# Kernel tuning notes

Measured on AMD Instinct MI355X. Metric: run time of the kernel, lower is better.

## Reference

```python
import jax, jax.numpy as jnp
import numpy as np

EPS = 1e-6
K = 20
NEG_SLOPE = 0.2

def knn_idx(x, k):
    # x: (B, D, N) flattened vector features; returns (B, N, k) neighbor indices
    inner = -2.0 * jnp.einsum('bdn,bdm->bnm', x, x)
    xx = jnp.sum(x * x, axis=1)  # (B, N)
    pd = -xx[:, :, None] - inner - xx[:, None, :]  # negative squared distance
    _, idx = jax.lax.top_k(pd, k)
    return idx

def get_graph_feature(x, k):
    # x: (B, C, 3, N) -> (B, 2C, 3, N, k) edge features (nbr - ctr, ctr)
    B, C, _, N = x.shape
    idx = knn_idx(x.reshape(B, C * 3, N), k)           # (B, N, k)
    feat = jnp.transpose(x, (0, 3, 1, 2))              # (B, N, C, 3)
    nb = jax.vmap(lambda f, i: f[i])(feat, idx)        # (B, N, k, C, 3)
    ctr = jnp.broadcast_to(feat[:, :, None], nb.shape)
    out = jnp.concatenate([nb - ctr, ctr], axis=3)     # (B, N, k, 2C, 3)
    return jnp.transpose(out, (0, 3, 4, 1, 2))

def vn_batchnorm(x, gamma, beta):
    # x: (B, C, 3, ...); BatchNorm (training stats) applied to vector norms
    norm = jnp.linalg.norm(x, axis=2) + EPS            # (B, C, ...)
    axes = (0,) + tuple(range(2, norm.ndim))
    mu = jnp.mean(norm, axis=axes, keepdims=True)
    var = jnp.var(norm, axis=axes, keepdims=True)
    shape = (1, -1) + (1,) * (norm.ndim - 2)
    nbn = (norm - mu) / jnp.sqrt(var + 1e-5) * gamma.reshape(shape) + beta.reshape(shape)
    return x / norm[:, :, None] * nbn[:, :, None]

def vn_linear_leakyrelu(x, w_feat, w_dir, gamma, beta):
    # x: (B, Cin, 3, ...) -> (B, Cout, 3, ...)
    p = jnp.einsum('oc,bc...->bo...', w_feat, x)
    p = vn_batchnorm(p, gamma, beta)
    d = jnp.einsum('oc,bc...->bo...', w_dir, x)
    dot = jnp.sum(p * d, axis=2, keepdims=True)
    dsq = jnp.sum(d * d, axis=2, keepdims=True)
    proj = p - (dot / (dsq + EPS)) * d
    return NEG_SLOPE * p + (1.0 - NEG_SLOPE) * jnp.where(dot >= 0, p, proj)

def _forward(x, w1, d1, g1, b1, w2, d2, g2, b2, w3, d3, g3, b3, w4, d4, g4, b4, w5, d5, g5, b5):
    h = jnp.transpose(x, (0, 2, 1))[:, None]           # (B, 1, 3, N)
    h = vn_linear_leakyrelu(get_graph_feature(h, K), w1, d1, g1, b1)
    x1 = jnp.mean(h, axis=-1)                          # mean_pool over k: (B, 21, 3, N)
    h = vn_linear_leakyrelu(get_graph_feature(x1, K), w2, d2, g2, b2)
    x2 = jnp.mean(h, axis=-1)                          # (B, 21, 3, N)
    h = vn_linear_leakyrelu(get_graph_feature(x2, K), w3, d3, g3, b3)
    x3 = jnp.mean(h, axis=-1)                          # (B, 42, 3, N)
    h = vn_linear_leakyrelu(get_graph_feature(x3, K), w4, d4, g4, b4)
    x4 = jnp.mean(h, axis=-1)                          # (B, 85, 3, N)
    cat = jnp.concatenate([x1, x2, x3, x4], axis=1)    # (B, 169, 3, N)
    return vn_linear_leakyrelu(cat, w5, d5, g5, b5)    # (B, 341, 3, N)

def setup_inputs():
    key = jax.random.key(0)
    B, N = 8, 1024
    d = {"x": jax.random.normal(key, (B, N, 3), dtype=jnp.float32)}
    feat_shapes = {"1": (21, 2), "2": (21, 42), "3": (42, 42), "4": (85, 84), "5": (341, 169)}
    dir_out = {"1": 21, "2": 21, "3": 42, "4": 85, "5": 1}  # conv5 shares nonlinearity -> 1 dir channel
    for i, (name, (co, ci)) in enumerate(feat_shapes.items()):
        k1, k2 = jax.random.split(jax.random.fold_in(key, i + 1))
        s = 1.0 / np.sqrt(ci)
        d["w" + name] = jax.random.uniform(k1, (co, ci), minval=-s, maxval=s, dtype=jnp.float32)
        d["d" + name] = jax.random.uniform(k2, (dir_out[name], ci), minval=-s, maxval=s, dtype=jnp.float32)
        d["g" + name] = jnp.ones((co,), dtype=jnp.float32)
        d["b" + name] = jnp.zeros((co,), dtype=jnp.float32)
    return d

def reference(x, w1, d1, g1, b1, w2, d2, g2, b2, w3, d3, g3, b3, w4, d4, g4, b4, w5, d5, g5, b5):
    return _forward(x, w1, d1, g1, b1, w2, d2, g2, b2, w3, d3, g3, b3, w4, d4, g4, b4, w5, d5, g5, b5)
```

## Files before the change

kernel.cpp:

```cpp
#include <hip/hip_runtime.h>
#include <math.h>

#define KNN 20
#define NS 0.2f
#define EPSV 1e-6f
#define QT 4
#define OT 8
#define CROW 507
#define SSPLIT 8

struct F3 { float x, y, z; };

extern __shared__ __align__(16) float smem[];

__global__ void k_transpose(const float* __restrict__ x, float* __restrict__ xt,
                            float* __restrict__ xx, int B, int N) {
    int i = blockIdx.x * blockDim.x + threadIdx.x;
    if (i >= B * N) return;
    int b = i / N, n = i % N;
    const float* src = x + (size_t)(b * N + n) * 3;
    float* dst = xt + (size_t)b * 3 * N + n;
    float s0 = src[0], s1 = src[1], s2 = src[2];
    dst[0] = s0;
    dst[(size_t)N] = s1;
    dst[(size_t)2 * N] = s2;
    float s = 0.f;
    s += s0 * s0;
    s += s1 * s1;
    s += s2 * s2;
    xx[i] = s;
}

__global__ void k_sqnorm(const float* __restrict__ X, float* __restrict__ xx,
                         int N, int D, long batchStride, long sliceOff) {
    int i = blockIdx.x * 256 + threadIdx.x;
    int b = i / N, n = i % N;
    const float* Xb = X + (size_t)b * batchStride + sliceOff + n;
    float s = 0.f;
    for (int d = 0; d < D; ++d) {
        float v = Xb[(size_t)d * N];
        s += v * v;
    }
    xx[i] = s;
}

__global__ void k_knn(const float* __restrict__ X, const float* __restrict__ xx,
                      int* __restrict__ idx,
                      int N, int D, long batchStride, long sliceOff) {
    int b = blockIdx.y;
    int q0 = blockIdx.x * QT;
    int tid = threadIdx.x;
    int lane = tid & 63;
    int wave = tid >> 6;

    __shared__ __align__(16) float qf[128 * QT];
    __shared__ __align__(16) float pd[QT][1024];

    const float* Xb = X + (size_t)b * batchStride + sliceOff;
    const float* xxb = xx + (size_t)b * N;

    for (int t = tid; t < QT * D; t += 256) {
        int d = t >> 2, q = t & 3;
        qf[d * QT + q] = Xb[(size_t)d * N + (q0 + q)];
    }
    __syncthreads();

    float a0x = 0.f, a0y = 0.f, a0z = 0.f, a0w = 0.f;
    float a1x = 0.f, a1y = 0.f, a1z = 0.f, a1w = 0.f;
    float a2x = 0.f, a2y = 0.f, a2z = 0.f, a2w = 0.f;
    float a3x = 0.f, a3y = 0.f, a3z = 0.f, a3w = 0.f;

    const float* mbase = Xb + 4 * tid;
#pragma unroll 3
    for (int d = 0; d < D; ++d) {
        float4 xm = *(const float4*)(mbase + (size_t)d * N);
        float4 qv = *(const float4*)(qf + d * QT);
        a0x += qv.x * xm.x; a0y += qv.x * xm.y; a0z += qv.x * xm.z; a0w += qv.x * xm.w;
        a1x += qv.y * xm.x; a1y += qv.y * xm.y; a1z += qv.y * xm.z; a1w += qv.y * xm.w;
        a2x += qv.z * xm.x; a2y += qv.z * xm.y; a2z += qv.z * xm.z; a2w += qv.z * xm.w;
        a3x += qv.w * xm.x; a3y += qv.w * xm.y; a3z += qv.w * xm.z; a3w += qv.w * xm.w;
    }

    {
        float4 m2 = *(const float4*)(xxb + 4 * tid);
        float4 qn = *(const float4*)(xxb + q0);
        float4 v;
        v.x = 2.f * a0x - qn.x - m2.x; v.y = 2.f * a0y - qn.x - m2.y;
        v.z = 2.f * a0z - qn.x - m2.z; v.w = 2.f * a0w - qn.x - m2.w;
        *(float4*)&pd[0][4 * tid] = v;
        v.x = 2.f * a1x - qn.y - m2.x; v.y = 2.f * a1y - qn.y - m2.y;
        v.z = 2.f * a1z - qn.y - m2.z; v.w = 2.f * a1w - qn.y - m2.w;
        *(float4*)&pd[1][4 * tid] = v;
        v.x = 2.f * a2x - qn.z - m2.x; v.y = 2.f * a2y - qn.z - m2.y;
        v.z = 2.f * a2z - qn.z - m2.z; v.w = 2.f * a2w - qn.z - m2.w;
        *(float4*)&pd[2][4 * tid] = v;
        v.x = 2.f * a3x - qn.w - m2.x; v.y = 2.f * a3y - qn.w - m2.y;
        v.z = 2.f * a3z - qn.w - m2.z; v.w = 2.f * a3w - qn.w - m2.w;
        *(float4*)&pd[3][4 * tid] = v;
    }
    __syncthreads();

    unsigned long long key[16];
#pragma unroll
    for (int t = 0; t < 16; ++t) {
        unsigned u = __float_as_uint(pd[wave][t * 64 + lane]);
        u ^= (unsigned)((int)u >> 31) | 0x80000000u;
        unsigned lo = (unsigned)(1023 - t * 64) - (unsigned)lane;
        key[t] = ((unsigned long long)u << 32) | (unsigned long long)lo;
    }

#define CE(a, b)                                        \
    {                                                   \
        unsigned long long ka = key[a], kb = key[b];    \
        bool sw = ka < kb;                              \
        key[a] = sw ? kb : ka;                          \
        key[b] = sw ? ka : kb;                          \
    }
    CE(0,1) CE(2,3) CE(4,5) CE(6,7) CE(8,9) CE(10,11) CE(12,13) CE(14,15)
    CE(0,2) CE(1,3) CE(4,6) CE(5,7) CE(8,10) CE(9,11) CE(12,14) CE(13,15)
    CE(1,2) CE(5,6) CE(9,10) CE(13,14)
    CE(0,4) CE(1,5) CE(2,6) CE(3,7) CE(8,12) CE(9,13) CE(10,14) CE(11,15)
    CE(2,4) CE(3,5) CE(10,12) CE(11,13)
    CE(1,2) CE(3,4) CE(5,6) CE(9,10) CE(11,12) CE(13,14)
    CE(0,8) CE(1,9) CE(2,10) CE(3,11) CE(4,12) CE(5,13) CE(6,14) CE(7,15)
    CE(4,8) CE(5,9) CE(6,10) CE(7,11)
    CE(2,4) CE(3,5) CE(6,8) CE(7,9) CE(10,12) CE(11,13)
    CE(1,2) CE(3,4) CE(5,6) CE(7,8) CE(9,10) CE(11,12) CE(13,14)
#undef CE

    long outBase = ((long)b * N + q0 + wave) * KNN;
    for (int it = 0; it < KNN; ++it) {
        unsigned long long bk = key[0];
#pragma unroll
        for (int off = 32; off >= 1; off >>= 1) {
            unsigned long long ok = __shfl_xor(bk, off, 64);
            if (ok > bk) bk = ok;
        }
        int bi = 1023 - (int)(bk & 1023u);
        if (lane == 0) idx[outBase + it] = bi;
        if ((bi & 63) == lane) {
#pragma unroll
            for (int t = 0; t < 15; ++t) key[t] = key[t + 1];
            key[15] = 0ull;
        }
    }
}

__global__ void k_matmul_pair_lds(const float* __restrict__ X, const float* __restrict__ W,
                                  const float* __restrict__ Dw,
                                  float* __restrict__ U, float* __restrict__ V,
                                  float* __restrict__ UD, float* __restrict__ VD,
                                  int C, int Co, int CoP, int TILE,
                                  int rowStride, int colOff) {
    const int CP = C * CoP;
    float* wts = smem;
    float* xs = smem + 4 * CP;

    int tid = threadIdx.x;
    int bn0 = blockIdx.x * TILE;
    int C3 = C * 3;

    int npad = CoP - Co;
    if (npad) {
        for (int t = tid; t < 4 * C * npad; t += 256) {
            int q = t / npad, oo = Co + t % npad;
            int mat = q / C, c = q % C;
            wts[mat * CP + c * CoP + oo] = 0.f;
        }
    }
    int twoCC = 2 * C * Co;
    for (int t = tid; t < twoCC; t += 256) {
        int o = t / (2 * C), c = t % (2 * C);
        float w = W[t], dw = Dw[t];
        if (c < C) {
            wts[c * CoP + o] = w;
            wts[2 * CP + c * CoP + o] = dw;
        } else {
            wts[CP + (c - C) * CoP + o] = w;
            wts[3 * CP + (c - C) * CoP + o] = dw;
        }
    }
    for (int t = tid; t < TILE * C3; t += 256) {
        int p = t / C3, cc = t % C3;
        xs[t] = X[(size_t)(bn0 + p) * rowStride + colOff + cc];
    }
    __syncthreads();
    for (int t = tid; t < CP; t += 256) {
        wts[CP + t] -= wts[t];
        wts[3 * CP + t] -= wts[2 * CP + t];
    }
    __syncthreads();

    int GPP = CoP >> 2;
    int items = TILE * GPP;
    for (int e = tid; e < items; e += 256) {
        int p = e / GPP, og = e - p * GPP;
        int o0 = og * 4;
        const float* xr = xs + p * C3;

        float aU[4][3], aV[4][3], aDu[4][3], aDv[4][3];
#pragma unroll
        for (int i = 0; i < 4; ++i)
#pragma unroll
            for (int j = 0; j < 3; ++j) {
                aU[i][j] = 0.f; aV[i][j] = 0.f; aDu[i][j] = 0.f; aDv[i][j] = 0.f;
            }

        for (int c = 0; c < C; ++c) {
            float x0 = xr[c * 3], x1 = xr[c * 3 + 1], x2 = xr[c * 3 + 2];
            const float* wp = wts + c * CoP + o0;
            float4 wa4 = *(const float4*)(wp);
            float4 wb4 = *(const float4*)(wp + CP);
            float4 da4 = *(const float4*)(wp + 2 * CP);
            float4 db4 = *(const float4*)(wp + 3 * CP);
            float wav[4] = {wa4.x, wa4.y, wa4.z, wa4.w};
            float wbv[4] = {wb4.x, wb4.y, wb4.z, wb4.w};
            float dav[4] = {da4.x, da4.y, da4.z, da4.w};
            float dbv[4] = {db4.x, db4.y, db4.z, db4.w};
#pragma unroll
            for (int i = 0; i < 4; ++i) {
                aU[i][0] += wav[i] * x0; aU[i][1] += wav[i] * x1; aU[i][2] += wav[i] * x2;
                aV[i][0] += wbv[i] * x0; aV[i][1] += wbv[i] * x1; aV[i][2] += wbv[i] * x2;
                aDu[i][0] += dav[i] * x0; aDu[i][1] += dav[i] * x1; aDu[i][2] += dav[i] * x2;
                aDv[i][0] += dbv[i] * x0; aDv[i][1] += dbv[i] * x1; aDv[i][2] += dbv[i] * x2;
            }
        }

        size_t base = ((size_t)(bn0 + p) * Co + o0) * 3;
#pragma unroll
        for (int i = 0; i < 4; ++i) {
            int o = o0 + i;
            if (o < Co) {
                size_t off = base + (size_t)i * 3;
                U[off] = aU[i][0]; U[off + 1] = aU[i][1]; U[off + 2] = aU[i][2];
                V[off] = aV[i][0]; V[off + 1] = aV[i][1]; V[off + 2] = aV[i][2];
                UD[off] = aDu[i][0]; UD[off + 1] = aDu[i][1]; UD[off + 2] = aDu[i][2];
                VD[off] = aDv[i][0]; VD[off + 1] = aDv[i][1]; VD[off + 2] = aDv[i][2];
            }
        }
    }
}

__global__ void k_stats_edge_det(const float* __restrict__ U, const float* __restrict__ V,
                                 const int* __restrict__ idx, float* __restrict__ partials,
                                 int N, int Co, int BN) {
    int o = blockIdx.x;
    int s = blockIdx.y;
    int tid = threadIdx.x;
    int P = BN / SSPLIT;
    int g0 = s * P;

    __shared__ float Ush[3072];
    __shared__ float r1[256], r2[256];

    for (int t = tid; t < P; t += 256) {
        F3 u3 = *(const F3*)(U + ((size_t)(g0 + t) * Co + o) * 3);
        Ush[t * 3 + 0] = u3.x;
        Ush[t * 3 + 1] = u3.y;
        Ush[t * 3 + 2] = u3.z;
    }
    __syncthreads();

    float s1 = 0.f, s2 = 0.f;
    for (int pl = tid; pl < P; pl += 256) {
        int g = g0 + pl;
        F3 v3 = *(const F3*)(V + ((size_t)g * Co + o) * 3);
        float v0 = v3.x, v1 = v3.y, v2 = v3.z;
        const int* ip = idx + (size_t)g * KNN;
        for (int kk = 0; kk < KNN; ++kk) {
            const float* Ur = Ush + ip[kk] * 3;
            float p0 = Ur[0] + v0;
            float p1 = Ur[1] + v1;
            float p2 = Ur[2] + v2;
            float nm = sqrtf(p0 * p0 + p1 * p1 + p2 * p2) + EPSV;
            s1 += nm;
            s2 += nm * nm;
        }
    }
    r1[tid] = s1; r2[tid] = s2;
    __syncthreads();
    for (int st = 128; st > 0; st >>= 1) {
        if (tid < st) { r1[tid] += r1[tid + st]; r2[tid] += r2[tid + st]; }
        __syncthreads();
    }
    if (tid == 0) {
        partials[(o * SSPLIT + s) * 2] = r1[0];
        partials[(o * SSPLIT + s) * 2 + 1] = r2[0];
    }
}

__global__ void k_final_edge_p(const float* __restrict__ U, const float* __restrict__ V,
                               const float* __restrict__ UD, const float* __restrict__ VD,
                               const int* __restrict__ idx, const float* __restrict__ partials,
                               const float* __restrict__ gamma, const float* __restrict__ beta,
                               float* __restrict__ catp,
                               int N, int Co, int colOff, float cnt, int total) {
    int g = blockIdx.x * 256 + threadIdx.x;
    if (g >= total) return;
    int o = g % Co;
    int r = g / Co;
    int n = r % N;
    int b = r / N;

    float s1 = 0.f, s2 = 0.f;
    for (int s = 0; s < SSPLIT; ++s) {
        s1 += partials[(o * SSPLIT + s) * 2];
        s2 += partials[(o * SSPLIT + s) * 2 + 1];
    }
    float mu = s1 / cnt;
    float var = s2 / cnt - mu * mu;
    float inv = rsqrtf(var + 1e-5f);
    float gmm = gamma[o], bt = beta[o];

    size_t ctr = ((size_t)(b * N + n) * Co + o) * 3;
    F3 vc = *(const F3*)(V + ctr);
    F3 wc = *(const F3*)(VD + ctr);
    float v0 = vc.x, v1 = vc.y, v2 = vc.z;
    float w0 = wc.x, w1 = wc.y, w2 = wc.z;
    const int* ip = idx + ((size_t)b * N + n) * KNN;

    float a0 = 0.f, a1 = 0.f, a2 = 0.f;
    for (int kk = 0; kk < KNN; ++kk) {
        int m = ip[kk];
        size_t nb = ((size_t)(b * N + m) * Co + o) * 3;
        F3 un = *(const F3*)(U + nb);
        F3 dn = *(const F3*)(UD + nb);
        float p0 = un.x + v0;
        float p1 = un.y + v1;
        float p2 = un.z + v2;
        float nm = sqrtf(p0 * p0 + p1 * p1 + p2 * p2) + EPSV;
        float nbn = (nm - mu) * inv * gmm + bt;
        float sc = nbn / nm;
        p0 *= sc; p1 *= sc; p2 *= sc;
        float d0 = dn.x + w0;
        float d1 = dn.y + w1;
        float d2 = dn.z + w2;
        float dot = p0 * d0 + p1 * d1 + p2 * d2;
        if (dot >= 0.f) {
            a0 += p0; a1 += p1; a2 += p2;
        } else {
            float f = dot / (d0 * d0 + d1 * d1 + d2 * d2 + EPSV);
            a0 += NS * p0 + (1.f - NS) * (p0 - f * d0);
            a1 += NS * p1 + (1.f - NS) * (p1 - f * d1);
            a2 += NS * p2 + (1.f - NS) * (p2 - f * d2);
        }
    }
    const float invk = 1.f / (float)KNN;
    float* outp = catp + (size_t)(b * N + n) * CROW + colOff + o * 3;
    outp[0] = a0 * invk;
    outp[1] = a1 * invk;
    outp[2] = a2 * invk;
}

__global__ void k_transpose_cat(const float* __restrict__ catp, float* __restrict__ catn,
                                int N, int c0, int CC) {
    __shared__ float tile[32][33];
    int b = blockIdx.z;
    int n0 = blockIdx.x * 32;
    int cb = blockIdx.y * 32;
    int tid = threadIdx.x;
    int tx = tid & 31, ty = tid >> 5;

#pragma unroll
    for (int rr = 0; rr < 4; ++rr) {
        int nl = ty + rr * 8;
        int c = cb + tx;
        if (c < CC)
            tile[nl][tx] = catp[(size_t)(b * N + n0 + nl) * CROW + c0 + c];
    }
    __syncthreads();
#pragma unroll
    for (int rr = 0; rr < 4; ++rr) {
        int cl = ty + rr * 8;
        int c = cb + cl;
        if (c < CC)
            catn[(size_t)b * CROW * N + (size_t)(c0 + c) * N + n0 + tx] = tile[tx][cl];
    }
}

__global__ void k_matmul_plain(const float* __restrict__ X, const float* __restrict__ W,
                               float* __restrict__ U,
                               int N, int Cin, int Cout, long batchStride, long sliceOff) {
    int ot = blockIdx.y;
    int b = blockIdx.z;
    int o0 = ot * OT;
    int tid = threadIdx.x;
    int n = blockIdx.x * 512 + 2 * tid;

    __shared__ __align__(16) float wsm[OT][176];
    for (int t = tid; t < OT * Cin; t += 256) {
        int oo = t / Cin, c = t % Cin;
        int o = o0 + oo;
        wsm[oo][c] = (o < Cout) ? W[(size_t)o * Cin + c] : 0.f;
    }
    __syncthreads();

    const float* Xp = X + (size_t)b * batchStride + sliceOff + n;
    float au[OT][3][2];
#pragma unroll
    for (int oo = 0; oo < OT; ++oo)
#pragma unroll
        for (int j = 0; j < 3; ++j) {
            au[oo][j][0] = 0.f; au[oo][j][1] = 0.f;
        }

    int c = 0;
    for (; c + 4 <= Cin; c += 4) {
        float2 xv[4][3];
#pragma unroll
        for (int cc = 0; cc < 4; ++cc)
#pragma unroll
            for (int j = 0; j < 3; ++j)
                xv[cc][j] = *(const float2*)(Xp + ((size_t)(c + cc) * 3 + j) * N);
#pragma unroll
        for (int oo = 0; oo < OT; ++oo) {
            float4 w4 = *(const float4*)&wsm[oo][c];
            float wv[4] = {w4.x, w4.y, w4.z, w4.w};
#pragma unroll
            for (int j = 0; j < 3; ++j) {
#pragma unroll
                for (int cc = 0; cc < 4; ++cc) {
                    au[oo][j][0] += wv[cc] * xv[cc][j].x;
                    au[oo][j][1] += wv[cc] * xv[cc][j].y;
                }
            }
        }
    }
    for (; c < Cin; ++c) {
        float2 xv[3];
#pragma unroll
        for (int j = 0; j < 3; ++j)
            xv[j] = *(const float2*)(Xp + ((size_t)c * 3 + j) * N);
#pragma unroll
        for (int oo = 0; oo < OT; ++oo) {
            float wv = wsm[oo][c];
#pragma unroll
            for (int j = 0; j < 3; ++j) {
                au[oo][j][0] += wv * xv[j].x;
                au[oo][j][1] += wv * xv[j].y;
            }
        }
    }
#pragma unroll
    for (int oo = 0; oo < OT; ++oo) {
        int o = o0 + oo;
        if (o < Cout) {
#pragma unroll
            for (int j = 0; j < 3; ++j) {
                float2 st; st.x = au[oo][j][0]; st.y = au[oo][j][1];
                *(float2*)&U[(((size_t)b * Cout + o) * 3 + j) * N + n] = st;
            }
        }
    }
}

__global__ void k_stats_plain_det(const float* __restrict__ U, float* __restrict__ mv,
                                  int N, int Cout, int BN, float cnt) {
    int o = blockIdx.x;
    int tid = threadIdx.x;
    float s1 = 0.f, s2 = 0.f;
    for (int g = tid; g < BN; g += 256) {
        int b = g / N, n = g % N;
        const float* Ub = U + (((size_t)b * Cout + o) * 3) * N;
        float p0 = Ub[n], p1 = Ub[(size_t)N + n], p2 = Ub[(size_t)2 * N + n];
        float nm = sqrtf(p0 * p0 + p1 * p1 + p2 * p2) + EPSV;
        s1 += nm;
        s2 += nm * nm;
    }
    __shared__ float r1[256], r2[256];
    r1[tid] = s1; r2[tid] = s2;
    __syncthreads();
    for (int st = 128; st > 0; st >>= 1) {
        if (tid < st) { r1[tid] += r1[tid + st]; r2[tid] += r2[tid + st]; }
        __syncthreads();
    }
    if (tid == 0) {
        float mu = r1[0] / cnt;
        float var = r2[0] / cnt - mu * mu;
        mv[2 * o] = mu;
        mv[2 * o + 1] = rsqrtf(var + 1e-5f);
    }
}

__global__ void k_final_plain(const float* __restrict__ U, const float* __restrict__ Dv,
                              const float* __restrict__ mv,
                              const float* __restrict__ gamma, const float* __restrict__ beta,
                              float* __restrict__ out, int N, int Cout) {
    int b = blockIdx.z, o = blockIdx.y, tid = threadIdx.x;
    int n = blockIdx.x * 256 + tid;
    float mu = mv[2 * o];
    float inv = mv[2 * o + 1];
    float g = gamma[o], bt = beta[o];

    const float* Ub = U + (((size_t)b * Cout + o) * 3) * N;
    float p0 = Ub[n], p1 = Ub[(size_t)N + n], p2 = Ub[(size_t)2 * N + n];
    float nm = sqrtf(p0 * p0 + p1 * p1 + p2 * p2) + EPSV;
    float nbn = (nm - mu) * inv * g + bt;
    float sc = nbn / nm;
    p0 *= sc; p1 *= sc; p2 *= sc;

    float d0 = Dv[((size_t)b * 3 + 0) * N + n];
    float d1 = Dv[((size_t)b * 3 + 1) * N + n];
    float d2 = Dv[((size_t)b * 3 + 2) * N + n];
    float dot = p0 * d0 + p1 * d1 + p2 * d2;
    float o0, o1, o2;
    if (dot >= 0.f) {
        o0 = p0; o1 = p1; o2 = p2;
    } else {
        float f = dot / (d0 * d0 + d1 * d1 + d2 * d2 + EPSV);
        o0 = NS * p0 + (1.f - NS) * (p0 - f * d0);
        o1 = NS * p1 + (1.f - NS) * (p1 - f * d1);
        o2 = NS * p2 + (1.f - NS) * (p2 - f * d2);
    }
    size_t ob = (((size_t)b * Cout + o) * 3) * N + n;
    out[ob] = o0;
    out[ob + (size_t)N] = o1;
    out[ob + (size_t)2 * N] = o2;
}

extern "C" void kernel_launch(void* const* d_in, const int* in_sizes, int n_in,
                              void* d_out, int out_size, void* d_ws, size_t ws_size,
                              hipStream_t stream) {
    (void)in_sizes; (void)n_in; (void)out_size; (void)ws_size;
    const int B = 8, N = 1024;

    const float* x = (const float*)d_in[0];
    const float* W[5]; const float* Dw[5]; const float* G[5]; const float* Bt[5];
    for (int l = 0; l < 5; ++l) {
        W[l]  = (const float*)d_in[1 + 4 * l];
        Dw[l] = (const float*)d_in[2 + 4 * l];
        G[l]  = (const float*)d_in[3 + 4 * l];
        Bt[l] = (const float*)d_in[4 + 4 * l];
    }

    float* ws = (float*)d_ws;
    size_t off = 0;
    float* xt = ws + off;     off += (size_t)B * 3 * N;
    int* idx = (int*)(ws + off); off += (size_t)B * N * KNN;
    float* catp = ws + off;   off += (size_t)B * N * CROW;
    float* catn = ws + off;   off += (size_t)B * N * CROW;
    float* Up = ws + off;     off += (size_t)B * N * 85 * 3;
    float* Vp = ws + off;     off += (size_t)B * N * 85 * 3;
    float* UDp = ws + off;    off += (size_t)B * N * 85 * 3;
    float* VDp = ws + off;    off += (size_t)B * N * 85 * 3;
    float* U5 = ws + off;     off += (size_t)B * 341 * 3 * N;
    float* d5buf = ws + off;  off += (size_t)B * 3 * N;
    float* xx = ws + off;     off += (size_t)B * N;
    float* partials = ws + off; off += (size_t)341 * SSPLIT * 2;
    float* mv = ws + off;     off += 2 * 341;

    k_transpose<<<(B * N + 255) / 256, 256, 0, stream>>>(x, xt, xx, B, N);

    const int Cin_[4]  = {1, 21, 21, 42};
    const int Cout_[4] = {21, 21, 42, 85};
    const int inOff_[4] = {-1, 0, 21, 42};
    const int outOff_[4] = {0, 21, 42, 84};
    const int Tile_[4] = {32, 32, 32, 8};

    const int BN = B * N;

    for (int l = 0; l < 4; ++l) {
        int C = Cin_[l], Co = Cout_[l];
        int D = C * 3;
        int CoP = (Co + 3) & ~3;
        int TILE = Tile_[l];

        const float* Xn; long bs, so;
        if (inOff_[l] < 0) { Xn = xt; bs = (long)3 * N; so = 0; }
        else { Xn = catn; bs = (long)CROW * N; so = (long)inOff_[l] * 3 * N; }

        const float* Xp; int rs, co;
        if (inOff_[l] < 0) { Xp = x; rs = 3; co = 0; }
        else { Xp = catp; rs = CROW; co = inOff_[l] * 3; }

        if (inOff_[l] >= 0)
            k_sqnorm<<<(B * N) / 256, 256, 0, stream>>>(Xn, xx, N, D, bs, so);

        dim3 gk(N / QT, B);
        k_knn<<<gk, 256, 0, stream>>>(Xn, xx, idx, N, D, bs, so);

        size_t smemB = (size_t)(4 * C * CoP + TILE * C * 3) * sizeof(float);
        k_matmul_pair_lds<<<(B * N) / TILE, 256, smemB, stream>>>(
            Xp, W[l], Dw[l], Up, Vp, UDp, VDp, C, Co, CoP, TILE, rs, co);

        dim3 gst(Co, SSPLIT);
        k_stats_edge_det<<<gst, 256, 0, stream>>>(Up, Vp, idx, partials, N, Co, BN);

        int total = BN * Co;
        k_final_edge_p<<<(total + 255) / 256, 256, 0, stream>>>(
            Up, Vp, UDp, VDp, idx, partials, G[l], Bt[l], catp,
            N, Co, outOff_[l] * 3, (float)((size_t)BN * KNN), total);

        int CC = Co * 3;
        dim3 gt(N / 32, (CC + 31) / 32, B);
        k_transpose_cat<<<gt, 256, 0, stream>>>(catp, catn, N, outOff_[l] * 3, CC);
    }

    {
        long bs = (long)CROW * N, so = 0;
        dim3 gm5(N / 512, (341 + OT - 1) / OT, B);
        k_matmul_plain<<<gm5, 256, 0, stream>>>(catn, W[4], U5, N, 169, 341, bs, so);
        dim3 gmd(N / 512, 1, B);
        k_matmul_plain<<<gmd, 256, 0, stream>>>(catn, Dw[4], d5buf, N, 169, 1, bs, so);
        k_stats_plain_det<<<341, 256, 0, stream>>>(U5, mv, N, 341, BN, (float)BN);
        dim3 gs5(N / 256, 341, B);
        k_final_plain<<<gs5, 256, 0, stream>>>(U5, d5buf, mv, G[4], Bt[4],
                                               (float*)d_out, N, 341);
    }
}
```

Measured before the change: 758.6 us.

## Fold sqnorm and final dir matmul into existing launches, spill knn keys to LDS

Removes the standalone squared-norm kernel by computing norms in extra blocks of the transpose kernel, reading the row-major cat buffer. Merges the single-channel direction matmul into the main final-layer matmul grid as an extra y-slice. In kNN selection, the upper half of each lane's sorted key list moves to shared memory and is refilled on demand, which cuts register pressure and shortens the shift chain. These changes cut launch count and registers, at the cost of extra branching and LDS traffic.

```diff
diff --git a/kernel.cpp b/kernel.cpp
--- a/kernel.cpp
+++ b/kernel.cpp
@@ -31,19 +31,6 @@
     xx[i] = s;
 }
 
-__global__ void k_sqnorm(const float* __restrict__ X, float* __restrict__ xx,
-                         int N, int D, long batchStride, long sliceOff) {
-    int i = blockIdx.x * 256 + threadIdx.x;
-    int b = i / N, n = i % N;
-    const float* Xb = X + (size_t)b * batchStride + sliceOff + n;
-    float s = 0.f;
-    for (int d = 0; d < D; ++d) {
-        float v = Xb[(size_t)d * N];
-        s += v * v;
-    }
-    xx[i] = s;
-}
-
 __global__ void k_knn(const float* __restrict__ X, const float* __restrict__ xx,
                       int* __restrict__ idx,
                       int N, int D, long batchStride, long sliceOff) {
@@ -128,6 +115,12 @@
     CE(1,2) CE(3,4) CE(5,6) CE(7,8) CE(9,10) CE(11,12) CE(13,14)
 #undef CE
 
+    __syncthreads();
+    unsigned long long* kl = (unsigned long long*)&pd[wave][0];
+#pragma unroll
+    for (int t = 8; t < 16; ++t) kl[(t - 8) * 64 + lane] = key[t];
+    int nspill = 0;
+
     long outBase = ((long)b * N + q0 + wave) * KNN;
     for (int it = 0; it < KNN; ++it) {
         unsigned long long bk = key[0];
@@ -139,9 +132,12 @@
         int bi = 1023 - (int)(bk & 1023u);
         if (lane == 0) idx[outBase + it] = bi;
         if ((bi & 63) == lane) {
-#pragma unroll
-            for (int t = 0; t < 15; ++t) key[t] = key[t + 1];
-            key[15] = 0ull;
+            key[0] = key[1]; key[1] = key[2]; key[2] = key[3]; key[3] = key[4];
+            key[4] = key[5]; key[5] = key[6]; key[6] = key[7];
+            int sidx = nspill < 8 ? nspill : 7;
+            unsigned long long nv = kl[sidx * 64 + lane];
+            key[7] = (nspill < 8) ? nv : 0ull;
+            nspill++;
         }
     }
 }
@@ -353,7 +349,22 @@
 }
 
 __global__ void k_transpose_cat(const float* __restrict__ catp, float* __restrict__ catn,
-                                int N, int c0, int CC) {
+                                int N, int c0, int CC,
+                                float* __restrict__ xx, int doSq) {
+    int ytiles = (CC + 31) >> 5;
+    if (doSq && (int)blockIdx.y == ytiles) {
+        if (blockIdx.z != 0) return;
+        int i = blockIdx.x * 256 + threadIdx.x;
+        const float* row = catp + (size_t)i * CROW + c0;
+        float s = 0.f;
+        for (int c = 0; c < CC; ++c) {
+            float v = row[c];
+            s += v * v;
+        }
+        xx[i] = s;
+        return;
+    }
+
     __shared__ float tile[32][33];
     int b = blockIdx.z;
     int n0 = blockIdx.x * 32;
@@ -379,19 +390,26 @@
 }
 
 __global__ void k_matmul_plain(const float* __restrict__ X, const float* __restrict__ W,
-                               float* __restrict__ U,
+                               const float* __restrict__ Dw,
+                               float* __restrict__ U, float* __restrict__ Ud,
                                int N, int Cin, int Cout, long batchStride, long sliceOff) {
     int ot = blockIdx.y;
     int b = blockIdx.z;
-    int o0 = ot * OT;
     int tid = threadIdx.x;
     int n = blockIdx.x * 512 + 2 * tid;
+
+    const float* Wp; float* Up; int CoutE; int o0;
+    if (ot == (int)gridDim.y - 1) {
+        Wp = Dw; Up = Ud; CoutE = 1; o0 = 0;
+    } else {
+        Wp = W; Up = U; CoutE = Cout; o0 = ot * OT;
+    }
 
     __shared__ __align__(16) float wsm[OT][176];
     for (int t = tid; t < OT * Cin; t += 256) {
         int oo = t / Cin, c = t % Cin;
         int o = o0 + oo;
-        wsm[oo][c] = (o < Cout) ? W[(size_t)o * Cin + c] : 0.f;
+        wsm[oo][c] = (o < CoutE) ? Wp[(size_t)o * Cin + c] : 0.f;
     }
     __syncthreads();
 
@@ -444,11 +462,11 @@
 #pragma unroll
     for (int oo = 0; oo < OT; ++oo) {
         int o = o0 + oo;
-        if (o < Cout) {
+        if (o < CoutE) {
 #pragma unroll
             for (int j = 0; j < 3; ++j) {
                 float2 st; st.x = au[oo][j][0]; st.y = au[oo][j][1];
-                *(float2*)&U[(((size_t)b * Cout + o) * 3 + j) * N + n] = st;
+                *(float2*)&Up[(((size_t)b * CoutE + o) * 3 + j) * N + n] = st;
             }
         }
     }
@@ -573,9 +591,6 @@
         if (inOff_[l] < 0) { Xp = x; rs = 3; co = 0; }
         else { Xp = catp; rs = CROW; co = inOff_[l] * 3; }
 
-        if (inOff_[l] >= 0)
-            k_sqnorm<<<(B * N) / 256, 256, 0, stream>>>(Xn, xx, N, D, bs, so);
-
         dim3 gk(N / QT, B);
         k_knn<<<gk, 256, 0, stream>>>(Xn, xx, idx, N, D, bs, so);
 
@@ -592,16 +607,16 @@
             N, Co, outOff_[l] * 3, (float)((size_t)BN * KNN), total);
 
         int CC = Co * 3;
-        dim3 gt(N / 32, (CC + 31) / 32, B);
-        k_transpose_cat<<<gt, 256, 0, stream>>>(catp, catn, N, outOff_[l] * 3, CC);
+        int doSq = (l < 3) ? 1 : 0;
+        dim3 gt(N / 32, (CC + 31) / 32 + doSq, B);
+        k_transpose_cat<<<gt, 256, 0, stream>>>(catp, catn, N, outOff_[l] * 3, CC, xx, doSq);
     }
 
     {
         long bs = (long)CROW * N, so = 0;
-        dim3 gm5(N / 512, (341 + OT - 1) / OT, B);
-        k_matmul_plain<<<gm5, 256, 0, stream>>>(catn, W[4], U5, N, 169, 341, bs, so);
-        dim3 gmd(N / 512, 1, B);
-        k_matmul_plain<<<gmd, 256, 0, stream>>>(catn, Dw[4], d5buf, N, 169, 1, bs, so);
+        dim3 gm5(N / 512, (341 + OT - 1) / OT + 1, B);
+        k_matmul_plain<<<gm5, 256, 0, stream>>>(catn, W[4], Dw[4], U5, d5buf,
+                                                N, 169, 341, bs, so);
         k_stats_plain_det<<<341, 256, 0, stream>>>(U5, mv, N, 341, BN, (float)BN);
         dim3 gs5(N / 256, 341, B);
         k_final_plain<<<gs5, 256, 0, stream>>>(U5, d5buf, mv, G[4], Bt[4],
```

Result: faster. 719.8 us (-5.1%).
